# Performance work log

Measured on AMD Instinct MI355X. Metric: run time of the kernel, lower is better.

The kernel has to match this reference:

```python
import jax, jax.numpy as jnp
import numpy as np

N = 100000          # nodes
E = 1600000         # edges
IN = 256            # in_feats
H = 4               # num_heads
D = 32              # out_feats
NEG_SLOPE = 0.2


def setup_inputs() -> dict:
    key = jax.random.key(0)
    k1, k2, k3, k4, k5, k6, k7 = jax.random.split(key, 7)
    feat = jax.random.normal(k1, (N, IN), dtype=jnp.float32)
    src = jax.random.randint(k2, (E,), 0, N, dtype=jnp.int64)
    dst = jax.random.randint(k3, (E,), 0, N, dtype=jnp.int64)
    # learned parameters (xavier-ish scale)
    fc_w = jax.random.normal(k4, (H * D, IN), dtype=jnp.float32) * (2.0 / (IN + H * D)) ** 0.5
    attn_l = jax.random.normal(k5, (1, H, D), dtype=jnp.float32) * 0.1
    attn_r = jax.random.normal(k6, (1, H, D), dtype=jnp.float32) * 0.1
    res_w = jax.random.normal(k7, (H * D, IN), dtype=jnp.float32) * (2.0 / (IN + H * D)) ** 0.5
    return {"feat": feat, "src": src, "dst": dst, "fc_w": fc_w,
            "attn_l": attn_l, "attn_r": attn_r, "res_w": res_w}


def reference(feat, src, dst, fc_w, attn_l, attn_r, res_w):
    # linear projection: [N, H, D]
    ft = (feat @ fc_w.T).reshape(N, H, D)
    # per-node attention logits: [N, H]
    el = jnp.sum(ft * attn_l, axis=-1)
    er = jnp.sum(ft * attn_r, axis=-1)
    # per-edge unnormalized attention (u_add_v + leaky_relu + exp): [E, H]
    e = el[src] + er[dst]
    e = jnp.where(e > 0, e, NEG_SLOPE * e)
    ex = jnp.exp(e)
    # edge-softmax denominator per destination node: [N, H]
    denom = jax.ops.segment_sum(ex, dst, num_segments=N)
    alpha = ex / denom[dst]                         # [E, H]
    # weighted scatter-add of source features: [N, H, D]
    msg = ft[src] * alpha[:, :, None]               # [E, H, D]
    agg = jax.ops.segment_sum(msg, dst, num_segments=N)
    # residual projection (res_fc is always applied in this module)
    res = (feat @ res_w.T).reshape(N, H, D)
    rst = agg + res
    return rst, agg  # (rst, dglrst)
```

## Files before the change

### kernel.cpp

```cpp
#include <hip/hip_runtime.h>
#include <hip/hip_bf16.h>
#include <cmath>

#define NNODES 100000
#define NEDGES 1600000
#define INF 256
#define HH 4
#define DD 32
#define HD 128
#define NEG_SLOPE 0.2f

typedef __attribute__((ext_vector_type(8))) short short8;
typedef __attribute__((ext_vector_type(4))) float f32x4;

#define GBM 64
#define GBK 64
__global__ __launch_bounds__(256) void gemm_kernel(const float* __restrict__ feat,
                                                   const float* __restrict__ fc_w,
                                                   const float* __restrict__ res_w,
                                                   const float* __restrict__ attn_l,
                                                   const float* __restrict__ attn_r,
                                                   __hip_bfloat16* __restrict__ ft,
                                                   float* __restrict__ out_rst,
                                                   float* __restrict__ el,
                                                   float* __restrict__ er) {
    __shared__ __align__(16) char Asm[GBM * GBK * 2];
    __shared__ __align__(16) char Bsm[256 * GBK * 2];

    const int tid  = threadIdx.x;
    const int lane = tid & 63;
    const int wc   = tid >> 6;
    const int lrow = lane & 15;
    const int lk   = lane >> 4;
    const int m0   = blockIdx.x * GBM;

    f32x4 acc[4][4];
#pragma unroll
    for (int m = 0; m < 4; ++m)
#pragma unroll
        for (int n = 0; n < 4; ++n) acc[m][n] = (f32x4){0.f, 0.f, 0.f, 0.f};

    for (int k0 = 0; k0 < INF; k0 += GBK) {
        if (k0) __syncthreads();
#pragma unroll
        for (int i = 0; i < 2; ++i) {
            int c   = tid + 256 * i;
            int row = c >> 3;
            int cb  = c & 7;
            int off = row * 128 + ((cb * 16) ^ ((row & 7) << 4));
            int grow = m0 + row;
            float4 f0 = make_float4(0.f, 0.f, 0.f, 0.f), f1 = f0;
            if (grow < NNODES) {
                const float* gp = &feat[(size_t)grow * INF + k0 + cb * 8];
                f0 = *(const float4*)gp;
                f1 = *(const float4*)(gp + 4);
            }
            union { short8 v; __hip_bfloat16 h[8]; } pk;
            pk.h[0] = __float2bfloat16(f0.x); pk.h[1] = __float2bfloat16(f0.y);
            pk.h[2] = __float2bfloat16(f0.z); pk.h[3] = __float2bfloat16(f0.w);
            pk.h[4] = __float2bfloat16(f1.x); pk.h[5] = __float2bfloat16(f1.y);
            pk.h[6] = __float2bfloat16(f1.z); pk.h[7] = __float2bfloat16(f1.w);
            *(short8*)(Asm + off) = pk.v;
        }
#pragma unroll
        for (int i = 0; i < 8; ++i) {
            int c   = tid + 256 * i;
            int row = c >> 3;
            int cb  = c & 7;
            int off = row * 128 + ((cb * 16) ^ ((row & 7) << 4));
            const float* wp = (row < 128) ? &fc_w[(size_t)row * 256]
                                          : &res_w[(size_t)(row - 128) * 256];
            float4 f0 = *(const float4*)&wp[k0 + cb * 8];
            float4 f1 = *(const float4*)&wp[k0 + cb * 8 + 4];
            union { short8 v; __hip_bfloat16 h[8]; } pk;
            pk.h[0] = __float2bfloat16(f0.x); pk.h[1] = __float2bfloat16(f0.y);
            pk.h[2] = __float2bfloat16(f0.z); pk.h[3] = __float2bfloat16(f0.w);
            pk.h[4] = __float2bfloat16(f1.x); pk.h[5] = __float2bfloat16(f1.y);
            pk.h[6] = __float2bfloat16(f1.z); pk.h[7] = __float2bfloat16(f1.w);
            *(short8*)(Bsm + off) = pk.v;
        }
        __syncthreads();
#pragma unroll
        for (int ks = 0; ks < 2; ++ks) {
            short8 a[4], b[4];
            int bc = ks * 64 + lk * 16;
#pragma unroll
            for (int m = 0; m < 4; ++m) {
                int row = m * 16 + lrow;
                a[m] = *(const short8*)(Asm + row * 128 + (bc ^ ((row & 7) << 4)));
            }
#pragma unroll
            for (int n = 0; n < 4; ++n) {
                int row = wc * 64 + n * 16 + lrow;
                b[n] = *(const short8*)(Bsm + row * 128 + (bc ^ ((row & 7) << 4)));
            }
#pragma unroll
            for (int m = 0; m < 4; ++m)
#pragma unroll
                for (int n = 0; n < 4; ++n)
                    acc[m][n] = __builtin_amdgcn_mfma_f32_16x16x32_bf16(a[m], b[n], acc[m][n], 0, 0, 0);
        }
    }

    float al[4], ar[4];
    if (wc < 2) {
#pragma unroll
        for (int n = 0; n < 4; ++n) {
            int col = wc * 64 + n * 16 + lrow;
            al[n] = attn_l[col];
            ar[n] = attn_r[col];
        }
    }
#pragma unroll
    for (int m = 0; m < 4; ++m) {
#pragma unroll
        for (int r = 0; r < 4; ++r) {
            int grow = m0 + m * 16 + lk * 4 + r;
            if (grow >= NNODES) continue;
            if (wc < 2) {
                float e_l0, e_l1, e_r0, e_r1;
                {
                    float v0 = acc[m][0][r], v1 = acc[m][1][r];
                    float v2 = acc[m][2][r], v3 = acc[m][3][r];
                    ft[(size_t)grow * HD + wc * 64 + 0 * 16 + lrow] = __float2bfloat16(v0);
                    ft[(size_t)grow * HD + wc * 64 + 1 * 16 + lrow] = __float2bfloat16(v1);
                    ft[(size_t)grow * HD + wc * 64 + 2 * 16 + lrow] = __float2bfloat16(v2);
                    ft[(size_t)grow * HD + wc * 64 + 3 * 16 + lrow] = __float2bfloat16(v3);
                    e_l0 = v0 * al[0] + v1 * al[1];
                    e_l1 = v2 * al[2] + v3 * al[3];
                    e_r0 = v0 * ar[0] + v1 * ar[1];
                    e_r1 = v2 * ar[2] + v3 * ar[3];
                }
#pragma unroll
                for (int msk = 1; msk < 16; msk <<= 1) {
                    e_l0 += __shfl_xor(e_l0, msk);
                    e_l1 += __shfl_xor(e_l1, msk);
                    e_r0 += __shfl_xor(e_r0, msk);
                    e_r1 += __shfl_xor(e_r1, msk);
                }
                if (lrow == 0) {
                    el[grow * HH + wc * 2 + 0] = e_l0;
                    el[grow * HH + wc * 2 + 1] = e_l1;
                    er[grow * HH + wc * 2 + 0] = e_r0;
                    er[grow * HH + wc * 2 + 1] = e_r1;
                }
            } else {
#pragma unroll
                for (int n = 0; n < 4; ++n) {
                    int col = wc * 64 + n * 16 + lrow - 128;
                    out_rst[(size_t)grow * HD + col] = acc[m][n][r];
                }
            }
        }
    }
}

__global__ void hist_kernel(const int* __restrict__ dst, int* __restrict__ deg) {
    int e = blockIdx.x * blockDim.x + threadIdx.x;
    if (e < NEDGES) atomicAdd(&deg[dst[e]], 1);
}

__global__ __launch_bounds__(256) void scan1_kernel(const int* __restrict__ deg,
                                                    int* __restrict__ excl,
                                                    int* __restrict__ blockSums) {
    __shared__ int sdata[256];
    int b = blockIdx.x, t = threadIdx.x;
    int base = b * 1024 + t * 4;
    int v[4];
#pragma unroll
    for (int i = 0; i < 4; ++i) {
        int idx = base + i;
        v[i] = (idx < NNODES) ? deg[idx] : 0;
    }
    int tsum = v[0] + v[1] + v[2] + v[3];
    sdata[t] = tsum;
    __syncthreads();
    for (int off = 1; off < 256; off <<= 1) {
        int x = (t >= off) ? sdata[t - off] : 0;
        __syncthreads();
        sdata[t] += x;
        __syncthreads();
    }
    int texcl = sdata[t] - tsum;
    if (t == 255) blockSums[b] = sdata[255];
    int run = texcl;
#pragma unroll
    for (int i = 0; i < 4; ++i) {
        int idx = base + i;
        if (idx < NNODES) excl[idx] = run;
        run += v[i];
    }
}

__global__ void scan2_kernel(int* __restrict__ blockSums, int nb) {
    __shared__ int sd[128];
    int t = threadIdx.x;
    int v = (t < nb) ? blockSums[t] : 0;
    sd[t] = v;
    __syncthreads();
    for (int off = 1; off < 128; off <<= 1) {
        int x = (t >= off) ? sd[t - off] : 0;
        __syncthreads();
        sd[t] += x;
        __syncthreads();
    }
    if (t < nb) blockSums[t] = sd[t] - v;
}

__global__ void scan3_kernel(int* __restrict__ excl, int* __restrict__ cursor,
                             const int* __restrict__ blockSums) {
    int idx = blockIdx.x * blockDim.x + threadIdx.x;
    if (idx < NNODES) {
        int v = excl[idx] + blockSums[idx >> 10];
        excl[idx] = v;
        cursor[idx] = v;
    }
}

__global__ void edge_kernel(const int* __restrict__ src, const int* __restrict__ dst,
                            int* __restrict__ cursor, int* __restrict__ csr_src) {
    int e = blockIdx.x * blockDim.x + threadIdx.x;
    if (e >= NEDGES) return;
    int s = src[e], d = dst[e];
    int pos = atomicAdd(&cursor[d], 1);
    csr_src[pos] = s;
}

__global__ __launch_bounds__(256) void agg_kernel(const int* __restrict__ offsets,
                                                  const int* __restrict__ deg,
                                                  const int* __restrict__ csr_src,
                                                  const float* __restrict__ el,
                                                  const float* __restrict__ er,
                                                  const ushort* __restrict__ ft2,
                                                  float* __restrict__ out_rst,
                                                  float* __restrict__ out_agg) {
    const int w = threadIdx.x >> 6;
    const int l = threadIdx.x & 63;
    const int n = blockIdx.x * 4 + w;
    if (n >= NNODES) return;
    const int start = offsets[n];
    const int dg    = deg[n];
    const int h     = l >> 4;
    const float ern = er[n * HH + h];

    float acc0 = 0.f, acc1 = 0.f, den = 0.f;

    for (int base = 0; base < dg; base += 16) {
        int eidx = base + (l & 15);
        int jc   = start + min(eidx, dg - 1);
        int sv   = csr_src[jc];
        float x  = el[sv * HH + h] + ern;
        x = (x > 0.f) ? x : NEG_SLOPE * x;
        float exS = (eidx < dg) ? expf(x) : 0.f;
#pragma unroll
        for (int e = 0; e < 16; ++e) {
            int   s  = __shfl(sv, e);
            float ex = __shfl(exS, (h << 4) | e);
            ushort2 u = *(const ushort2*)&ft2[((size_t)s << 7) + (l << 1)];
            float f0, f1;
            {
                union { unsigned int i; float f; } c0, c1;
                c0.i = ((unsigned int)u.x) << 16;
                c1.i = ((unsigned int)u.y) << 16;
                f0 = c0.f; f1 = c1.f;
            }
            acc0 += ex * f0;
            acc1 += ex * f1;
            den  += ex;
        }
    }

    float a0 = (dg > 0) ? acc0 / den : 0.f;
    float a1 = (dg > 0) ? acc1 / den : 0.f;
    size_t o = (size_t)n * HD + (l << 1);
    *(float2*)&out_agg[o] = make_float2(a0, a1);
    float2 rr = *(const float2*)&out_rst[o];
    *(float2*)&out_rst[o] = make_float2(rr.x + a0, rr.y + a1);
}

extern "C" void kernel_launch(void* const* d_in, const int* in_sizes, int n_in,
                              void* d_out, int out_size, void* d_ws, size_t ws_size,
                              hipStream_t stream) {
    const float* feat   = (const float*)d_in[0];
    const int*   src    = (const int*)d_in[1];
    const int*   dst    = (const int*)d_in[2];
    const float* fc_w   = (const float*)d_in[3];
    const float* attn_l = (const float*)d_in[4];
    const float* attn_r = (const float*)d_in[5];
    const float* res_w  = (const float*)d_in[6];

    float* out_rst = (float*)d_out;
    float* out_agg = out_rst + (size_t)NNODES * HD;

    char* p = (char*)d_ws;
    auto alloc = [&](size_t bytes) {
        char* r = p;
        p += (bytes + 255) & ~(size_t)255;
        return (void*)r;
    };
    __hip_bfloat16* ft = (__hip_bfloat16*)alloc((size_t)NNODES * HD * 2);
    float* el        = (float*)alloc((size_t)NNODES * HH * 4);
    float* er        = (float*)alloc((size_t)NNODES * HH * 4);
    int*   deg       = (int*)alloc((size_t)NNODES * 4);
    int*   offsets   = (int*)alloc((size_t)NNODES * 4);
    int*   cursor    = (int*)alloc((size_t)NNODES * 4);
    int*   blockSums = (int*)alloc(1024);
    int*   csr_src   = (int*)alloc((size_t)NEDGES * 4);

    const int nb_scan = (NNODES + 1023) / 1024;

    hipMemsetAsync(deg, 0, (size_t)NNODES * 4, stream);

    gemm_kernel<<<(NNODES + GBM - 1) / GBM, 256, 0, stream>>>(
        feat, fc_w, res_w, attn_l, attn_r, ft, out_rst, el, er);
    hist_kernel<<<(NEDGES + 255) / 256, 256, 0, stream>>>(dst, deg);
    scan1_kernel<<<nb_scan, 256, 0, stream>>>(deg, offsets, blockSums);
    scan2_kernel<<<1, 128, 0, stream>>>(blockSums, nb_scan);
    scan3_kernel<<<(NNODES + 255) / 256, 256, 0, stream>>>(offsets, cursor, blockSums);
    edge_kernel<<<(NEDGES + 255) / 256, 256, 0, stream>>>(src, dst, cursor, csr_src);
    agg_kernel<<<(NNODES + 3) / 4, 256, 0, stream>>>(offsets, deg, csr_src, el, er,
                                                     (const ushort*)ft, out_rst, out_agg);
}
```

Baseline: 521.8 us.

## Bucket edges by 64-node destination blocks and aggregate with shared-memory atomics

Replaces the full per-node CSR build (histogram, three-stage scan, per-node scatter) with a coarse bucketing of edges into 64-node destination blocks. Each bucket is split into 8 sub-buckets to spread contention, and the scan shrinks to one single-block kernel. Aggregation then runs one workgroup per 64-node block, accumulating softmax-weighted features and denominators with LDS float atomics before writing normalized results. This cuts the scan and scatter cost and the per-node degree imbalance. In exchange it stores (src,dst) pairs at 8 bytes per edge, adds heavy LDS atomic traffic and 33KB of shared memory per block, and makes the floating-point summation order nondeterministic.

Result: slower. 1.666 ms (+219.2%).

```diff
diff --git a/kernel.cpp b/kernel.cpp
--- a/kernel.cpp
+++ b/kernel.cpp
@@ -10,8 +10,18 @@
 #define HD 128
 #define NEG_SLOPE 0.2f
 
+#define NB 1563
+#define NBG (NB * 8)
+#define EBLK 6250
+
 typedef __attribute__((ext_vector_type(8))) short short8;
 typedef __attribute__((ext_vector_type(4))) float f32x4;
+
+__device__ __forceinline__ float bf2f(ushort u) {
+    union { unsigned int i; float f; } c;
+    c.i = ((unsigned int)u) << 16;
+    return c.f;
+}
 
 #define GBM 64
 #define GBK 64
@@ -155,127 +165,128 @@
     }
 }
 
-__global__ void hist_kernel(const int* __restrict__ dst, int* __restrict__ deg) {
-    int e = blockIdx.x * blockDim.x + threadIdx.x;
-    if (e < NEDGES) atomicAdd(&deg[dst[e]], 1);
-}
-
-__global__ __launch_bounds__(256) void scan1_kernel(const int* __restrict__ deg,
-                                                    int* __restrict__ excl,
-                                                    int* __restrict__ blockSums) {
-    __shared__ int sdata[256];
-    int b = blockIdx.x, t = threadIdx.x;
-    int base = b * 1024 + t * 4;
-    int v[4];
-#pragma unroll
-    for (int i = 0; i < 4; ++i) {
+__global__ void bhist_kernel(const int* __restrict__ dst, int* __restrict__ bcount) {
+    int e = blockIdx.x * 256 + threadIdx.x;
+    int d = dst[e];
+    atomicAdd(&bcount[(d >> 6) * 8 + (blockIdx.x & 7)], 1);
+}
+
+__global__ __launch_bounds__(1024) void bscan_kernel(int* __restrict__ a) {
+    __shared__ int part[1024];
+    const int t = threadIdx.x;
+    const int CH = (NBG + 1023) / 1024;
+    int v[CH];
+    int base = t * CH;
+    int s = 0;
+#pragma unroll
+    for (int i = 0; i < CH; ++i) {
         int idx = base + i;
-        v[i] = (idx < NNODES) ? deg[idx] : 0;
-    }
-    int tsum = v[0] + v[1] + v[2] + v[3];
-    sdata[t] = tsum;
+        v[i] = (idx < NBG) ? a[idx] : 0;
+        s += v[i];
+    }
+    part[t] = s;
     __syncthreads();
-    for (int off = 1; off < 256; off <<= 1) {
-        int x = (t >= off) ? sdata[t - off] : 0;
+    for (int off = 1; off < 1024; off <<= 1) {
+        int x = (t >= off) ? part[t - off] : 0;
         __syncthreads();
-        sdata[t] += x;
+        part[t] += x;
         __syncthreads();
     }
-    int texcl = sdata[t] - tsum;
-    if (t == 255) blockSums[b] = sdata[255];
-    int run = texcl;
-#pragma unroll
-    for (int i = 0; i < 4; ++i) {
+    int run = part[t] - s;
+#pragma unroll
+    for (int i = 0; i < CH; ++i) {
         int idx = base + i;
-        if (idx < NNODES) excl[idx] = run;
+        if (idx < NBG) a[idx] = run;
         run += v[i];
     }
-}
-
-__global__ void scan2_kernel(int* __restrict__ blockSums, int nb) {
-    __shared__ int sd[128];
-    int t = threadIdx.x;
-    int v = (t < nb) ? blockSums[t] : 0;
-    sd[t] = v;
+    if (t == 1023) a[NBG] = run;
+}
+
+__global__ void bscatter_kernel(const int* __restrict__ src, const int* __restrict__ dst,
+                                int* __restrict__ bcursor, int2* __restrict__ bedges) {
+    int e = blockIdx.x * 256 + threadIdx.x;
+    int s = src[e], d = dst[e];
+    int pos = atomicAdd(&bcursor[(d >> 6) * 8 + (blockIdx.x & 7)], 1);
+    bedges[pos] = make_int2(s, d);
+}
+
+__global__ __launch_bounds__(256) void agg2_kernel(const int* __restrict__ boff,
+                                                   const int2* __restrict__ bedges,
+                                                   const float* __restrict__ el,
+                                                   const float* __restrict__ er,
+                                                   const ushort* __restrict__ ft2,
+                                                   float* __restrict__ out_rst,
+                                                   float* __restrict__ out_agg) {
+    __shared__ float acc_s[64 * 128];
+    __shared__ float den_s[64 * 4];
+    __shared__ float er_s[64 * 4];
+    const int tid   = threadIdx.x;
+    const int b     = blockIdx.x;
+    const int node0 = b << 6;
+
+    for (int i = tid; i < 64 * 128; i += 256) acc_s[i] = 0.f;
+    den_s[tid] = 0.f;
+    {
+        int n = node0 + (tid >> 2);
+        er_s[tid] = (n < NNODES) ? er[n * HH + (tid & 3)] : 0.f;
+    }
     __syncthreads();
-    for (int off = 1; off < 128; off <<= 1) {
-        int x = (t >= off) ? sd[t - off] : 0;
-        __syncthreads();
-        sd[t] += x;
-        __syncthreads();
-    }
-    if (t < nb) blockSums[t] = sd[t] - v;
-}
-
-__global__ void scan3_kernel(int* __restrict__ excl, int* __restrict__ cursor,
-                             const int* __restrict__ blockSums) {
-    int idx = blockIdx.x * blockDim.x + threadIdx.x;
-    if (idx < NNODES) {
-        int v = excl[idx] + blockSums[idx >> 10];
-        excl[idx] = v;
-        cursor[idx] = v;
-    }
-}
-
-__global__ void edge_kernel(const int* __restrict__ src, const int* __restrict__ dst,
-                            int* __restrict__ cursor, int* __restrict__ csr_src) {
-    int e = blockIdx.x * blockDim.x + threadIdx.x;
-    if (e >= NEDGES) return;
-    int s = src[e], d = dst[e];
-    int pos = atomicAdd(&cursor[d], 1);
-    csr_src[pos] = s;
-}
-
-__global__ __launch_bounds__(256) void agg_kernel(const int* __restrict__ offsets,
-                                                  const int* __restrict__ deg,
-                                                  const int* __restrict__ csr_src,
-                                                  const float* __restrict__ el,
-                                                  const float* __restrict__ er,
-                                                  const ushort* __restrict__ ft2,
-                                                  float* __restrict__ out_rst,
-                                                  float* __restrict__ out_agg) {
-    const int w = threadIdx.x >> 6;
-    const int l = threadIdx.x & 63;
-    const int n = blockIdx.x * 4 + w;
-    if (n >= NNODES) return;
-    const int start = offsets[n];
-    const int dg    = deg[n];
-    const int h     = l >> 4;
-    const float ern = er[n * HH + h];
-
-    float acc0 = 0.f, acc1 = 0.f, den = 0.f;
-
-    for (int base = 0; base < dg; base += 16) {
-        int eidx = base + (l & 15);
-        int jc   = start + min(eidx, dg - 1);
-        int sv   = csr_src[jc];
-        float x  = el[sv * HH + h] + ern;
-        x = (x > 0.f) ? x : NEG_SLOPE * x;
-        float exS = (eidx < dg) ? expf(x) : 0.f;
-#pragma unroll
-        for (int e = 0; e < 16; ++e) {
-            int   s  = __shfl(sv, e);
-            float ex = __shfl(exS, (h << 4) | e);
-            ushort2 u = *(const ushort2*)&ft2[((size_t)s << 7) + (l << 1)];
-            float f0, f1;
-            {
-                union { unsigned int i; float f; } c0, c1;
-                c0.i = ((unsigned int)u.x) << 16;
-                c1.i = ((unsigned int)u.y) << 16;
-                f0 = c0.f; f1 = c1.f;
-            }
-            acc0 += ex * f0;
-            acc1 += ex * f1;
-            den  += ex;
-        }
-    }
-
-    float a0 = (dg > 0) ? acc0 / den : 0.f;
-    float a1 = (dg > 0) ? acc1 / den : 0.f;
-    size_t o = (size_t)n * HD + (l << 1);
-    *(float2*)&out_agg[o] = make_float2(a0, a1);
-    float2 rr = *(const float2*)&out_rst[o];
-    *(float2*)&out_rst[o] = make_float2(rr.x + a0, rr.y + a1);
+
+    const int bstart = boff[b * 8];
+    const int bend   = boff[(b + 1) * 8];
+    const int wv = tid >> 6, l = tid & 63;
+    const int h  = l >> 4;
+    const int c0 = l << 1;
+
+    for (int base = bstart + wv * 4; base < bend; base += 16) {
+        int last = bend - 1;
+        int2 e0 = bedges[base];
+        int2 e1 = bedges[min(base + 1, last)];
+        int2 e2 = bedges[min(base + 2, last)];
+        int2 e3 = bedges[min(base + 3, last)];
+        float x0 = el[e0.x * HH + h] + er_s[(e0.y & 63) * 4 + h];
+        float x1 = el[e1.x * HH + h] + er_s[(e1.y & 63) * 4 + h];
+        float x2 = el[e2.x * HH + h] + er_s[(e2.y & 63) * 4 + h];
+        float x3 = el[e3.x * HH + h] + er_s[(e3.y & 63) * 4 + h];
+        x0 = (x0 > 0.f) ? x0 : NEG_SLOPE * x0;
+        x1 = (x1 > 0.f) ? x1 : NEG_SLOPE * x1;
+        x2 = (x2 > 0.f) ? x2 : NEG_SLOPE * x2;
+        x3 = (x3 > 0.f) ? x3 : NEG_SLOPE * x3;
+        float ex0 = __expf(x0);
+        float ex1 = (base + 1 < bend) ? __expf(x1) : 0.f;
+        float ex2 = (base + 2 < bend) ? __expf(x2) : 0.f;
+        float ex3 = (base + 3 < bend) ? __expf(x3) : 0.f;
+        ushort2 u0 = *(const ushort2*)&ft2[((size_t)e0.x << 7) + c0];
+        ushort2 u1 = *(const ushort2*)&ft2[((size_t)e1.x << 7) + c0];
+        ushort2 u2 = *(const ushort2*)&ft2[((size_t)e2.x << 7) + c0];
+        ushort2 u3 = *(const ushort2*)&ft2[((size_t)e3.x << 7) + c0];
+        atomicAdd(&acc_s[(e0.y & 63) * 128 + c0    ], ex0 * bf2f(u0.x));
+        atomicAdd(&acc_s[(e0.y & 63) * 128 + c0 + 1], ex0 * bf2f(u0.y));
+        atomicAdd(&acc_s[(e1.y & 63) * 128 + c0    ], ex1 * bf2f(u1.x));
+        atomicAdd(&acc_s[(e1.y & 63) * 128 + c0 + 1], ex1 * bf2f(u1.y));
+        atomicAdd(&acc_s[(e2.y & 63) * 128 + c0    ], ex2 * bf2f(u2.x));
+        atomicAdd(&acc_s[(e2.y & 63) * 128 + c0 + 1], ex2 * bf2f(u2.y));
+        atomicAdd(&acc_s[(e3.y & 63) * 128 + c0    ], ex3 * bf2f(u3.x));
+        atomicAdd(&acc_s[(e3.y & 63) * 128 + c0 + 1], ex3 * bf2f(u3.y));
+        if ((l & 15) == 0) {
+            atomicAdd(&den_s[(e0.y & 63) * 4 + h], ex0);
+            atomicAdd(&den_s[(e1.y & 63) * 4 + h], ex1);
+            atomicAdd(&den_s[(e2.y & 63) * 4 + h], ex2);
+            atomicAdd(&den_s[(e3.y & 63) * 4 + h], ex3);
+        }
+    }
+    __syncthreads();
+
+    const int c = tid & 127;
+    for (int nl = tid >> 7; nl < 64; nl += 2) {
+        int n = node0 + nl;
+        if (n >= NNODES) break;
+        float d = den_s[nl * 4 + (c >> 5)];
+        float a = (d > 0.f) ? acc_s[nl * 128 + c] / d : 0.f;
+        size_t o = ((size_t)n << 7) + c;
+        out_agg[o] = a;
+        out_rst[o] += a;
+    }
 }
 
 extern "C" void kernel_launch(void* const* d_in, const int* in_sizes, int n_in,
@@ -299,25 +310,20 @@
         return (void*)r;
     };
     __hip_bfloat16* ft = (__hip_bfloat16*)alloc((size_t)NNODES * HD * 2);
-    float* el        = (float*)alloc((size_t)NNODES * HH * 4);
-    float* er        = (float*)alloc((size_t)NNODES * HH * 4);
-    int*   deg       = (int*)alloc((size_t)NNODES * 4);
-    int*   offsets   = (int*)alloc((size_t)NNODES * 4);
-    int*   cursor    = (int*)alloc((size_t)NNODES * 4);
-    int*   blockSums = (int*)alloc(1024);
-    int*   csr_src   = (int*)alloc((size_t)NEDGES * 4);
-
-    const int nb_scan = (NNODES + 1023) / 1024;
-
-    hipMemsetAsync(deg, 0, (size_t)NNODES * 4, stream);
+    float* el       = (float*)alloc((size_t)NNODES * HH * 4);
+    float* er       = (float*)alloc((size_t)NNODES * HH * 4);
+    int*   bcount   = (int*)alloc((size_t)(NBG + 1) * 4);
+    int*   bcursor  = (int*)alloc((size_t)NBG * 4);
+    int2*  bedges   = (int2*)alloc((size_t)NEDGES * 8);
+
+    hipMemsetAsync(bcount, 0, (size_t)(NBG + 1) * 4, stream);
 
     gemm_kernel<<<(NNODES + GBM - 1) / GBM, 256, 0, stream>>>(
         feat, fc_w, res_w, attn_l, attn_r, ft, out_rst, el, er);
-    hist_kernel<<<(NEDGES + 255) / 256, 256, 0, stream>>>(dst, deg);
-    scan1_kernel<<<nb_scan, 256, 0, stream>>>(deg, offsets, blockSums);
-    scan2_kernel<<<1, 128, 0, stream>>>(blockSums, nb_scan);
-    scan3_kernel<<<(NNODES + 255) / 256, 256, 0, stream>>>(offsets, cursor, blockSums);
-    edge_kernel<<<(NEDGES + 255) / 256, 256, 0, stream>>>(src, dst, cursor, csr_src);
-    agg_kernel<<<(NNODES + 3) / 4, 256, 0, stream>>>(offsets, deg, csr_src, el, er,
-                                                     (const ushort*)ft, out_rst, out_agg);
-}
+    bhist_kernel<<<EBLK, 256, 0, stream>>>(dst, bcount);
+    bscan_kernel<<<1, 1024, 0, stream>>>(bcount);
+    hipMemcpyAsync(bcursor, bcount, (size_t)NBG * 4, hipMemcpyDeviceToDevice, stream);
+    bscatter_kernel<<<EBLK, 256, 0, stream>>>(src, dst, bcursor, bedges);
+    agg2_kernel<<<NB, 256, 0, stream>>>(bcount, bedges, el, er,
+                                        (const ushort*)ft, out_rst, out_agg);
+}
```
